# Performance work log

Hardware: AMD Instinct MI355X
Metric: run time of the kernel (lower is better)

Reference implementation:

```python
import jax, jax.numpy as jnp
import numpy as np

B, S, H = 2, 2048, 2048
NQ, NKV = 32, 8
HD = H // NQ  # 64


def setup_inputs() -> dict:
    key = jax.random.key(0)
    ks = jax.random.split(key, 9)
    s = 1.0 / np.sqrt(H)
    return {
        "x": jax.random.normal(ks[0], (B, S, H), dtype=jnp.float32),
        "Wq": jax.random.normal(ks[1], (H, H), dtype=jnp.float32) * s,
        "bq": jnp.zeros((H,), dtype=jnp.float32),
        "Wk": jax.random.normal(ks[2], (H, NKV * HD), dtype=jnp.float32) * s,
        "bk": jnp.zeros((NKV * HD,), dtype=jnp.float32),
        "Wv": jax.random.normal(ks[3], (H, NKV * HD), dtype=jnp.float32) * s,
        "bv": jnp.zeros((NKV * HD,), dtype=jnp.float32),
        "Wo": jax.random.normal(ks[4], (H, H), dtype=jnp.float32) * s,
        "bo": jnp.zeros((H,), dtype=jnp.float32),
    }


def reference(x, Wq, bq, Wk, bk, Wv, bv, Wo, bo):
    Bx, Sx, _ = x.shape
    g = NQ // NKV  # queries per kv head
    q = (x @ Wq + bq).reshape(Bx, Sx, NKV, g, HD)   # grouped query heads
    k = (x @ Wk + bk).reshape(Bx, Sx, NKV, HD)
    v = (x @ Wv + bv).reshape(Bx, Sx, NKV, HD)
    # scores: [B, NKV, g, S, S] -- broadcast KV across group instead of jnp.repeat
    scores = jnp.einsum('bshgd,bkhd->bhgsk', q, k) / jnp.sqrt(jnp.float32(HD))
    probs = jax.nn.softmax(scores, axis=-1)
    out = jnp.einsum('bhgsk,bkhd->bshgd', probs, v).reshape(Bx, Sx, H)
    return out @ Wo + bo
```

## Files before the change

### kernel.cpp

```cpp
#include <hip/hip_runtime.h>
#include <cstdint>
#include <cstddef>

typedef unsigned short u16;
typedef __bf16 bf16x8 __attribute__((ext_vector_type(8)));
typedef float f32x4 __attribute__((ext_vector_type(4)));
typedef unsigned short u16x4 __attribute__((ext_vector_type(4)));
typedef unsigned short u16x8 __attribute__((ext_vector_type(8)));
typedef uint32_t u32x4 __attribute__((ext_vector_type(4)));
typedef __attribute__((address_space(1))) unsigned int as1_uint;
typedef __attribute__((address_space(3))) unsigned int as3_uint;

__device__ __forceinline__ u16 f2bf(float f) {
  uint32_t u = __builtin_bit_cast(uint32_t, f);
  u += 0x7FFFu + ((u >> 16) & 1u);
  return (u16)(u >> 16);
}

__device__ __forceinline__ uint32_t cvtpk2bf(float a, float b) {
  uint32_t r;
  asm("v_cvt_pk_bf16_f32 %0, %1, %2" : "=v"(r) : "v"(a), "v"(b));
  return r;
}

__device__ __forceinline__ float max3f(float a, float b, float c) {
  return fmaxf(fmaxf(a, b), c);
}

__device__ __forceinline__ void gld_lds16(const void* g, void* l) {
  __builtin_amdgcn_global_load_lds((as1_uint*)g, (as3_uint*)l, 16, 0, 0);
}

__global__ __launch_bounds__(256) void k_prep(const float* __restrict__ x,
                                              u16* __restrict__ xb,
                                              const float* __restrict__ Wq,
                                              const float* __restrict__ Wk,
                                              const float* __restrict__ Wv,
                                              const float* __restrict__ Wo,
                                              u16* __restrict__ wqkvT,
                                              u16* __restrict__ woT) {
  constexpr int K = 2048;
  const int z = blockIdx.z;
  if (z >= 4) {
    int i = ((z - 4) * 1024 + blockIdx.y * 32 + blockIdx.x) * 256 + threadIdx.x;
    const float4* p = reinterpret_cast<const float4*>(x) + (size_t)i * 2;
    float4 a = p[0], b = p[1];
    u16x8 r;
    r[0] = f2bf(a.x); r[1] = f2bf(a.y); r[2] = f2bf(a.z); r[3] = f2bf(a.w);
    r[4] = f2bf(b.x); r[5] = f2bf(b.y); r[6] = f2bf(b.z); r[7] = f2bf(b.w);
    *reinterpret_cast<u16x8*>(xb + (size_t)i * 8) = r;
    return;
  }
  const float* W; u16* Wt; int N;
  if (z == 0)      { W = Wq; Wt = wqkvT;                        N = 2048; }
  else if (z == 1) { W = Wo; Wt = woT;                          N = 2048; }
  else if (z == 2) { W = Wk; Wt = wqkvT + (size_t)2048 * 2048;  N = 512;  }
  else             { W = Wv; Wt = wqkvT + (size_t)2560 * 2048;  N = 512;  }
  const int n0 = blockIdx.x * 64;
  if (n0 >= N) return;
  __shared__ u16 tile[64][72];
  const int k0 = blockIdx.y * 64;
  const int r = threadIdx.x >> 4;
  const int c4 = (threadIdx.x & 15) * 4;
#pragma unroll
  for (int i = 0; i < 4; ++i) {
    int kk = r + i * 16;
    float4 v = *reinterpret_cast<const float4*>(W + (size_t)(k0 + kk) * N + n0 + c4);
    tile[kk][c4 + 0] = f2bf(v.x); tile[kk][c4 + 1] = f2bf(v.y);
    tile[kk][c4 + 2] = f2bf(v.z); tile[kk][c4 + 3] = f2bf(v.w);
  }
  __syncthreads();
#pragma unroll
  for (int i = 0; i < 4; ++i) {
    int nn = r + i * 16;
    u16x4 o;
    o[0] = tile[c4 + 0][nn]; o[1] = tile[c4 + 1][nn];
    o[2] = tile[c4 + 2][nn]; o[3] = tile[c4 + 3][nn];
    *reinterpret_cast<u16x4*>(Wt + (size_t)(n0 + nn) * K + k0 + c4) = o;
  }
}

template <bool F32OUT>
__global__ __launch_bounds__(256) void k_gemm(const u16* __restrict__ A,
                                              const u16* __restrict__ Bt,
                                              const float* __restrict__ b0,
                                              const float* __restrict__ b1,
                                              const float* __restrict__ b2,
                                              void* __restrict__ Cout,
                                              int M, int N, int K,
                                              int n1, int n2,
                                              int scaleN, float scaleV,
                                              u16* __restrict__ vout, int vcol0, int ldC) {
  __shared__ __align__(16) u16 As[128 * 64];
  __shared__ __align__(16) u16 Bs[128 * 64];
  const int id = blockIdx.y * gridDim.x + blockIdx.x;
  const int cpx = (gridDim.x * gridDim.y) >> 3;
  const int nid = (id & 7) * cpx + (id >> 3);
  const int m0 = (nid / gridDim.x) * 128, n0 = (nid % gridDim.x) * 128;
  const int tid = threadIdx.x;
  const int l = tid & 63, w = tid >> 6;
  const int wm = w >> 1, wn = w & 1;
  const int lr = l & 15, lo = l >> 4;
  const int srow = w * 8 + (l >> 3);
  const int sc = (l & 7) ^ ((l >> 3) & 7);
  f32x4 acc[4][4] = {};
  for (int kt = 0; kt < K; kt += 64) {
    __syncthreads();
#pragma unroll
    for (int it = 0; it < 4; ++it) {
      int row = it * 32 + srow;
      gld_lds16(A + (size_t)(m0 + row) * K + kt + sc * 8,
                (char*)As + (it * 32 + w * 8) * 128);
      gld_lds16(Bt + (size_t)(n0 + row) * K + kt + sc * 8,
                (char*)Bs + (it * 32 + w * 8) * 128);
    }
    __syncthreads();
    bf16x8 af[4][2], bfr[4][2];
#pragma unroll
    for (int mi = 0; mi < 4; ++mi) {
      int row = wm * 64 + mi * 16 + lr;
#pragma unroll
      for (int ks = 0; ks < 2; ++ks) {
        int ch = (ks * 4 + lo) ^ (row & 7);
        af[mi][ks] = *reinterpret_cast<const bf16x8*>((const char*)As + row * 128 + ch * 16);
      }
    }
#pragma unroll
    for (int nj = 0; nj < 4; ++nj) {
      int row = wn * 64 + nj * 16 + lr;
#pragma unroll
      for (int ks = 0; ks < 2; ++ks) {
        int ch = (ks * 4 + lo) ^ (row & 7);
        bfr[nj][ks] = *reinterpret_cast<const bf16x8*>((const char*)Bs + row * 128 + ch * 16);
      }
    }
#pragma unroll
    for (int mi = 0; mi < 4; ++mi)
#pragma unroll
      for (int nj = 0; nj < 4; ++nj) {
        acc[mi][nj] = __builtin_amdgcn_mfma_f32_16x16x32_bf16(af[mi][0], bfr[nj][0], acc[mi][nj], 0, 0, 0);
        acc[mi][nj] = __builtin_amdgcn_mfma_f32_16x16x32_bf16(af[mi][1], bfr[nj][1], acc[mi][nj], 0, 0, 0);
      }
  }
#pragma unroll
  for (int mi = 0; mi < 4; ++mi) {
    int row = m0 + wm * 64 + mi * 16 + lo * 4;
#pragma unroll
    for (int nj = 0; nj < 4; ++nj) {
      int col = n0 + wn * 64 + nj * 16 + lr;
      float bv = (col < n1) ? b0[col] : (col < n2 ? b1[col - n1] : b2[col - n2]);
      float scc = (col < scaleN) ? scaleV : 1.0f;
      float v[4];
#pragma unroll
      for (int r = 0; r < 4; ++r) v[r] = (acc[mi][nj][r] + bv) * scc;
      if (!F32OUT && col >= vcol0) {
        int d = col - vcol0;
        int kvh = d >> 6, dcol = d & 63;
        int bb = row >> 11, token = row & 2047;
        u16x4 o;
#pragma unroll
        for (int r = 0; r < 4; ++r) o[r] = f2bf(v[r]);
        *reinterpret_cast<u16x4*>(vout + (((size_t)(bb * 8 + kvh) * 64 + dcol) * 2048 + token)) = o;
      } else {
#pragma unroll
        for (int r = 0; r < 4; ++r) {
          if (F32OUT) ((float*)Cout)[(size_t)(row + r) * ldC + col] = v[r];
          else        ((u16*)Cout)[(size_t)(row + r) * ldC + col] = f2bf(v[r]);
        }
      }
    }
  }
}

__global__ __launch_bounds__(512, 4) void k_attn(const u16* __restrict__ QKV,
                                                 const u16* __restrict__ VT,
                                                 u16* __restrict__ Oa) {
  constexpr int S = 2048, LDQ = 2560;
  constexpr float THR = 8.0f;
  __shared__ __align__(16) u16 Ks[2][64 * 64];
  __shared__ __align__(16) u16 Vs[2][64 * 64];
  const int qt = blockIdx.x, h = blockIdx.y, b = blockIdx.z;
  const int kvh = h >> 2;
  const int tid = threadIdx.x, l = tid & 63, w = tid >> 6;
  const int lr = l & 15, lo = l >> 4;
  const size_t base = (size_t)b * S * LDQ;
  const u16* Qg = QKV + base + h * 64;
  const u16* Kg = QKV + base + 2048 + kvh * 64;
  const u16* Vg = VT + (size_t)(b * 8 + kvh) * 64 * 2048;
  const int qrow = qt * 128 + w * 16 + lr;
  const bf16x8 aq0 = *reinterpret_cast<const bf16x8*>(Qg + (size_t)qrow * LDQ + lo * 8);
  const bf16x8 aq1 = *reinterpret_cast<const bf16x8*>(Qg + (size_t)qrow * LDQ + 32 + lo * 8);
  u32x4 onesw; onesw[0] = 0x3F803F80u; onesw[1] = 0x3F803F80u; onesw[2] = 0x3F803F80u; onesw[3] = 0x3F803F80u;
  const bf16x8 ones = __builtin_bit_cast(bf16x8, onesw);
  f32x4 acc[4] = {};
  f32x4 lsum4 = {};
  float mrun = -1e30f;
  const int krow = tid >> 3;
  const int ksc = (l & 7) ^ ((l >> 3) & 7);
  gld_lds16(Kg + (size_t)krow * LDQ + ksc * 8, (char*)Ks[0] + (w * 8) * 128);
  gld_lds16(Vg + (size_t)krow * 2048 + ksc * 8, (char*)Vs[0] + (w * 8) * 128);
  int cur = 0;
  for (int kt = 0; kt < S; kt += 64) {
    __syncthreads();
    if (kt + 64 < S) {
      const int nb = cur ^ 1, nk = kt + 64;
      gld_lds16(Kg + (size_t)(nk + krow) * LDQ + ksc * 8, (char*)Ks[nb] + (w * 8) * 128);
      gld_lds16(Vg + (size_t)krow * 2048 + nk + ksc * 8, (char*)Vs[nb] + (w * 8) * 128);
    }
    float p[16];
    const u16* KsC = Ks[cur];
    __builtin_amdgcn_s_setprio(1);
#pragma unroll
    for (int t = 0; t < 4; ++t) {
      const int row = t * 16 + lr;
      bf16x8 k0 = *reinterpret_cast<const bf16x8*>((const char*)KsC + row * 128 + ((lo ^ (row & 7)) * 16));
      bf16x8 k1 = *reinterpret_cast<const bf16x8*>((const char*)KsC + row * 128 + (((4 + lo) ^ (row & 7)) * 16));
      f32x4 zz = {};
      zz = __builtin_amdgcn_mfma_f32_16x16x32_bf16(k0, aq0, zz, 0, 0, 0);
      zz = __builtin_amdgcn_mfma_f32_16x16x32_bf16(k1, aq1, zz, 0, 0, 0);
#pragma unroll
      for (int r = 0; r < 4; ++r) p[t * 4 + r] = zz[r];
    }
    __builtin_amdgcn_s_setprio(0);
    float m0 = max3f(p[0], p[1], p[2]);
    float m1 = max3f(p[3], p[4], p[5]);
    float m2 = max3f(p[6], p[7], p[8]);
    float m3 = max3f(p[9], p[10], p[11]);
    float m4 = max3f(p[12], p[13], p[14]);
    float tm = fmaxf(max3f(m0, m1, m2), max3f(m3, m4, p[15]));
    tm = fmaxf(tm, __shfl_xor(tm, 16, 64));
    tm = fmaxf(tm, __shfl_xor(tm, 32, 64));
    if (__all(tm <= mrun + THR)) {
#pragma unroll
      for (int i = 0; i < 16; ++i) p[i] = __builtin_amdgcn_exp2f(p[i] - mrun);
    } else {
      float mnew = fmaxf(mrun, tm);
      float alpha = __builtin_amdgcn_exp2f(mrun - mnew);
      mrun = mnew;
#pragma unroll
      for (int i = 0; i < 16; ++i) p[i] = __builtin_amdgcn_exp2f(p[i] - mnew);
#pragma unroll
      for (int r = 0; r < 4; ++r) {
        float ar = __shfl(alpha, lo * 4 + r, 64);
        lsum4[r] *= ar;
#pragma unroll
        for (int nj = 0; nj < 4; ++nj) acc[nj][r] *= ar;
      }
    }
    uint32_t w00 = cvtpk2bf(p[0], p[1]),   w01 = cvtpk2bf(p[2], p[3]);
    uint32_t w10 = cvtpk2bf(p[4], p[5]),   w11 = cvtpk2bf(p[6], p[7]);
    uint32_t w20 = cvtpk2bf(p[8], p[9]),   w21 = cvtpk2bf(p[10], p[11]);
    uint32_t w30 = cvtpk2bf(p[12], p[13]), w31 = cvtpk2bf(p[14], p[15]);
    asm volatile("v_permlane32_swap_b32 %0, %1" : "+v"(w00), "+v"(w10));
    asm volatile("v_permlane16_swap_b32 %0, %1" : "+v"(w00), "+v"(w10));
    asm volatile("v_permlane32_swap_b32 %0, %1" : "+v"(w01), "+v"(w11));
    asm volatile("v_permlane16_swap_b32 %0, %1" : "+v"(w01), "+v"(w11));
    asm volatile("v_permlane32_swap_b32 %0, %1" : "+v"(w20), "+v"(w30));
    asm volatile("v_permlane16_swap_b32 %0, %1" : "+v"(w20), "+v"(w30));
    asm volatile("v_permlane32_swap_b32 %0, %1" : "+v"(w21), "+v"(w31));
    asm volatile("v_permlane16_swap_b32 %0, %1" : "+v"(w21), "+v"(w31));
    u32x4 pq0; pq0[0] = w00; pq0[1] = w01; pq0[2] = w10; pq0[3] = w11;
    u32x4 pq1; pq1[0] = w20; pq1[1] = w21; pq1[2] = w30; pq1[3] = w31;
    const bf16x8 pa0 = __builtin_bit_cast(bf16x8, pq0);
    const bf16x8 pa1 = __builtin_bit_cast(bf16x8, pq1);
    const u16* VsC = Vs[cur];
    __builtin_amdgcn_s_setprio(1);
    lsum4 = __builtin_amdgcn_mfma_f32_16x16x32_bf16(pa0, ones, lsum4, 0, 0, 0);
    lsum4 = __builtin_amdgcn_mfma_f32_16x16x32_bf16(pa1, ones, lsum4, 0, 0, 0);
#pragma unroll
    for (int nj = 0; nj < 4; ++nj) {
      const int vr = nj * 16 + lr;
      const bf16x8 bv0 = *reinterpret_cast<const bf16x8*>((const char*)VsC + vr * 128 + ((lo ^ (vr & 7)) * 16));
      const bf16x8 bv1 = *reinterpret_cast<const bf16x8*>((const char*)VsC + vr * 128 + (((4 + lo) ^ (vr & 7)) * 16));
      acc[nj] = __builtin_amdgcn_mfma_f32_16x16x32_bf16(pa0, bv0, acc[nj], 0, 0, 0);
      acc[nj] = __builtin_amdgcn_mfma_f32_16x16x32_bf16(pa1, bv1, acc[nj], 0, 0, 0);
    }
    __builtin_amdgcn_s_setprio(0);
    cur ^= 1;
  }
  float lf[4];
#pragma unroll
  for (int r = 0; r < 4; ++r) lf[r] = 1.0f / lsum4[r];
  const size_t orow = (size_t)b * S + qt * 128 + w * 16 + lo * 4;
#pragma unroll
  for (int nj = 0; nj < 4; ++nj) {
    const int col = h * 64 + nj * 16 + lr;
#pragma unroll
    for (int r = 0; r < 4; ++r)
      Oa[(orow + r) * 2048 + col] = f2bf(acc[nj][r] * lf[r]);
  }
}

extern "C" void kernel_launch(void* const* d_in, const int* in_sizes, int n_in,
                              void* d_out, int out_size, void* d_ws, size_t ws_size,
                              hipStream_t stream) {
  const float* x  = (const float*)d_in[0];
  const float* Wq = (const float*)d_in[1];
  const float* bq = (const float*)d_in[2];
  const float* Wk = (const float*)d_in[3];
  const float* bk = (const float*)d_in[4];
  const float* Wv = (const float*)d_in[5];
  const float* bv = (const float*)d_in[6];
  const float* Wo = (const float*)d_in[7];
  const float* bo = (const float*)d_in[8];
  float* out = (float*)d_out;
  char* ws = (char*)d_ws;

  u16*   xb    = (u16*)(ws + 0);
  u16*   wqkvT = (u16*)(ws + 16777216);
  u16*   woT   = (u16*)(ws + 29360128);
  u16*   qkv   = (u16*)(ws + 37748736);
  u16*   attn  = (u16*)(ws + 58720256);
  u16*   vtg   = (u16*)(ws + 75497472);

  const float SCL = 0.125f * 1.44269504088896341f;

  k_prep<<<dim3(32, 32, 8), 256, 0, stream>>>(x, xb, Wq, Wk, Wv, Wo, wqkvT, woT);
  k_gemm<false><<<dim3(24, 32), 256, 0, stream>>>(xb, wqkvT, bq, bk, bv, qkv,
                                                  4096, 3072, 2048, 2048, 2560, 2048, SCL,
                                                  vtg, 2560, 2560);
  k_attn<<<dim3(16, 32, 2), 512, 0, stream>>>(qkv, vtg, attn);
  k_gemm<true><<<dim3(16, 32), 256, 0, stream>>>(attn, woT, bo, bo, bo, out,
                                                 4096, 2048, 2048, 2048, 4096, 0, 1.0f,
                                                 nullptr, 1 << 30, 2048);
}
```

Measured before the change: 253.3 us.

## Process 128-key tiles per attention iteration instead of 64

The attention loop now stages two 64-key K/V sub-tiles per double-buffered stage and processes 128 keys per iteration. This halves the number of barriers, online-softmax max reductions and rescale checks per key, and gives more independent MFMA work per iteration. In exchange it doubles LDS use and register pressure, and the launch bounds drop to 2 blocks per CU, which may reduce occupancy and latency hiding.

```diff
diff --git a/kernel.cpp b/kernel.cpp
--- a/kernel.cpp
+++ b/kernel.cpp
@@ -172,13 +172,13 @@
   }
 }
 
-__global__ __launch_bounds__(512, 4) void k_attn(const u16* __restrict__ QKV,
+__global__ __launch_bounds__(512, 2) void k_attn(const u16* __restrict__ QKV,
                                                  const u16* __restrict__ VT,
                                                  u16* __restrict__ Oa) {
   constexpr int S = 2048, LDQ = 2560;
   constexpr float THR = 8.0f;
-  __shared__ __align__(16) u16 Ks[2][64 * 64];
-  __shared__ __align__(16) u16 Vs[2][64 * 64];
+  __shared__ __align__(16) u16 Ks[2][2][64 * 64];
+  __shared__ __align__(16) u16 Vs[2][2][64 * 64];
   const int qt = blockIdx.x, h = blockIdx.y, b = blockIdx.z;
   const int kvh = h >> 2;
   const int tid = threadIdx.x, l = tid & 63, w = tid >> 6;
@@ -197,48 +197,69 @@
   float mrun = -1e30f;
   const int krow = tid >> 3;
   const int ksc = (l & 7) ^ ((l >> 3) & 7);
-  gld_lds16(Kg + (size_t)krow * LDQ + ksc * 8, (char*)Ks[0] + (w * 8) * 128);
-  gld_lds16(Vg + (size_t)krow * 2048 + ksc * 8, (char*)Vs[0] + (w * 8) * 128);
+  gld_lds16(Kg + (size_t)krow * LDQ + ksc * 8,           (char*)Ks[0][0] + (w * 8) * 128);
+  gld_lds16(Kg + (size_t)(64 + krow) * LDQ + ksc * 8,    (char*)Ks[0][1] + (w * 8) * 128);
+  gld_lds16(Vg + (size_t)krow * 2048 + ksc * 8,          (char*)Vs[0][0] + (w * 8) * 128);
+  gld_lds16(Vg + (size_t)krow * 2048 + 64 + ksc * 8,     (char*)Vs[0][1] + (w * 8) * 128);
   int cur = 0;
-  for (int kt = 0; kt < S; kt += 64) {
+  for (int kt = 0; kt < S; kt += 128) {
     __syncthreads();
-    if (kt + 64 < S) {
-      const int nb = cur ^ 1, nk = kt + 64;
-      gld_lds16(Kg + (size_t)(nk + krow) * LDQ + ksc * 8, (char*)Ks[nb] + (w * 8) * 128);
-      gld_lds16(Vg + (size_t)krow * 2048 + nk + ksc * 8, (char*)Vs[nb] + (w * 8) * 128);
-    }
-    float p[16];
-    const u16* KsC = Ks[cur];
+    if (kt + 128 < S) {
+      const int nb = cur ^ 1, nk = kt + 128;
+      gld_lds16(Kg + (size_t)(nk + krow) * LDQ + ksc * 8,        (char*)Ks[nb][0] + (w * 8) * 128);
+      gld_lds16(Kg + (size_t)(nk + 64 + krow) * LDQ + ksc * 8,   (char*)Ks[nb][1] + (w * 8) * 128);
+      gld_lds16(Vg + (size_t)krow * 2048 + nk + ksc * 8,         (char*)Vs[nb][0] + (w * 8) * 128);
+      gld_lds16(Vg + (size_t)krow * 2048 + nk + 64 + ksc * 8,    (char*)Vs[nb][1] + (w * 8) * 128);
+    }
+    float p0[16], p1[16];
+    const u16* K0 = Ks[cur][0];
+    const u16* K1 = Ks[cur][1];
     __builtin_amdgcn_s_setprio(1);
 #pragma unroll
     for (int t = 0; t < 4; ++t) {
       const int row = t * 16 + lr;
-      bf16x8 k0 = *reinterpret_cast<const bf16x8*>((const char*)KsC + row * 128 + ((lo ^ (row & 7)) * 16));
-      bf16x8 k1 = *reinterpret_cast<const bf16x8*>((const char*)KsC + row * 128 + (((4 + lo) ^ (row & 7)) * 16));
-      f32x4 zz = {};
-      zz = __builtin_amdgcn_mfma_f32_16x16x32_bf16(k0, aq0, zz, 0, 0, 0);
-      zz = __builtin_amdgcn_mfma_f32_16x16x32_bf16(k1, aq1, zz, 0, 0, 0);
-#pragma unroll
-      for (int r = 0; r < 4; ++r) p[t * 4 + r] = zz[r];
+      const int c0 = (lo ^ (row & 7)) * 16, c1 = ((4 + lo) ^ (row & 7)) * 16;
+      bf16x8 k00 = *reinterpret_cast<const bf16x8*>((const char*)K0 + row * 128 + c0);
+      bf16x8 k01 = *reinterpret_cast<const bf16x8*>((const char*)K0 + row * 128 + c1);
+      bf16x8 k10 = *reinterpret_cast<const bf16x8*>((const char*)K1 + row * 128 + c0);
+      bf16x8 k11 = *reinterpret_cast<const bf16x8*>((const char*)K1 + row * 128 + c1);
+      f32x4 z0 = {}, z1 = {};
+      z0 = __builtin_amdgcn_mfma_f32_16x16x32_bf16(k00, aq0, z0, 0, 0, 0);
+      z0 = __builtin_amdgcn_mfma_f32_16x16x32_bf16(k01, aq1, z0, 0, 0, 0);
+      z1 = __builtin_amdgcn_mfma_f32_16x16x32_bf16(k10, aq0, z1, 0, 0, 0);
+      z1 = __builtin_amdgcn_mfma_f32_16x16x32_bf16(k11, aq1, z1, 0, 0, 0);
+#pragma unroll
+      for (int r = 0; r < 4; ++r) { p0[t * 4 + r] = z0[r]; p1[t * 4 + r] = z1[r]; }
     }
     __builtin_amdgcn_s_setprio(0);
-    float m0 = max3f(p[0], p[1], p[2]);
-    float m1 = max3f(p[3], p[4], p[5]);
-    float m2 = max3f(p[6], p[7], p[8]);
-    float m3 = max3f(p[9], p[10], p[11]);
-    float m4 = max3f(p[12], p[13], p[14]);
-    float tm = fmaxf(max3f(m0, m1, m2), max3f(m3, m4, p[15]));
-    tm = fmaxf(tm, __shfl_xor(tm, 16, 64));
-    tm = fmaxf(tm, __shfl_xor(tm, 32, 64));
+    float a0 = max3f(p0[0], p0[1], p0[2]);
+    float a1 = max3f(p0[3], p0[4], p0[5]);
+    float a2 = max3f(p0[6], p0[7], p0[8]);
+    float a3 = max3f(p0[9], p0[10], p0[11]);
+    float a4 = max3f(p0[12], p0[13], p0[14]);
+    float tm0 = fmaxf(max3f(a0, a1, a2), max3f(a3, a4, p0[15]));
+    float b0m = max3f(p1[0], p1[1], p1[2]);
+    float b1m = max3f(p1[3], p1[4], p1[5]);
+    float b2m = max3f(p1[6], p1[7], p1[8]);
+    float b3m = max3f(p1[9], p1[10], p1[11]);
+    float b4m = max3f(p1[12], p1[13], p1[14]);
+    float tm1 = fmaxf(max3f(b0m, b1m, b2m), max3f(b3m, b4m, p1[15]));
+    tm0 = fmaxf(tm0, __shfl_xor(tm0, 16, 64));
+    tm1 = fmaxf(tm1, __shfl_xor(tm1, 16, 64));
+    tm0 = fmaxf(tm0, __shfl_xor(tm0, 32, 64));
+    tm1 = fmaxf(tm1, __shfl_xor(tm1, 32, 64));
+    float tm = fmaxf(tm0, tm1);
     if (__all(tm <= mrun + THR)) {
 #pragma unroll
-      for (int i = 0; i < 16; ++i) p[i] = __builtin_amdgcn_exp2f(p[i] - mrun);
+      for (int i = 0; i < 16; ++i) { p0[i] = __builtin_amdgcn_exp2f(p0[i] - mrun);
+                                     p1[i] = __builtin_amdgcn_exp2f(p1[i] - mrun); }
     } else {
       float mnew = fmaxf(mrun, tm);
       float alpha = __builtin_amdgcn_exp2f(mrun - mnew);
       mrun = mnew;
 #pragma unroll
-      for (int i = 0; i < 16; ++i) p[i] = __builtin_amdgcn_exp2f(p[i] - mnew);
+      for (int i = 0; i < 16; ++i) { p0[i] = __builtin_amdgcn_exp2f(p0[i] - mnew);
+                                     p1[i] = __builtin_amdgcn_exp2f(p1[i] - mnew); }
 #pragma unroll
       for (int r = 0; r < 4; ++r) {
         float ar = __shfl(alpha, lo * 4 + r, 64);
@@ -247,10 +268,14 @@
         for (int nj = 0; nj < 4; ++nj) acc[nj][r] *= ar;
       }
     }
-    uint32_t w00 = cvtpk2bf(p[0], p[1]),   w01 = cvtpk2bf(p[2], p[3]);
-    uint32_t w10 = cvtpk2bf(p[4], p[5]),   w11 = cvtpk2bf(p[6], p[7]);
-    uint32_t w20 = cvtpk2bf(p[8], p[9]),   w21 = cvtpk2bf(p[10], p[11]);
-    uint32_t w30 = cvtpk2bf(p[12], p[13]), w31 = cvtpk2bf(p[14], p[15]);
+    uint32_t w00 = cvtpk2bf(p0[0], p0[1]),   w01 = cvtpk2bf(p0[2], p0[3]);
+    uint32_t w10 = cvtpk2bf(p0[4], p0[5]),   w11 = cvtpk2bf(p0[6], p0[7]);
+    uint32_t w20 = cvtpk2bf(p0[8], p0[9]),   w21 = cvtpk2bf(p0[10], p0[11]);
+    uint32_t w30 = cvtpk2bf(p0[12], p0[13]), w31 = cvtpk2bf(p0[14], p0[15]);
+    uint32_t x00 = cvtpk2bf(p1[0], p1[1]),   x01 = cvtpk2bf(p1[2], p1[3]);
+    uint32_t x10 = cvtpk2bf(p1[4], p1[5]),   x11 = cvtpk2bf(p1[6], p1[7]);
+    uint32_t x20 = cvtpk2bf(p1[8], p1[9]),   x21 = cvtpk2bf(p1[10], p1[11]);
+    uint32_t x30 = cvtpk2bf(p1[12], p1[13]), x31 = cvtpk2bf(p1[14], p1[15]);
     asm volatile("v_permlane32_swap_b32 %0, %1" : "+v"(w00), "+v"(w10));
     asm volatile("v_permlane16_swap_b32 %0, %1" : "+v"(w00), "+v"(w10));
     asm volatile("v_permlane32_swap_b32 %0, %1" : "+v"(w01), "+v"(w11));
@@ -259,21 +284,41 @@
     asm volatile("v_permlane16_swap_b32 %0, %1" : "+v"(w20), "+v"(w30));
     asm volatile("v_permlane32_swap_b32 %0, %1" : "+v"(w21), "+v"(w31));
     asm volatile("v_permlane16_swap_b32 %0, %1" : "+v"(w21), "+v"(w31));
+    asm volatile("v_permlane32_swap_b32 %0, %1" : "+v"(x00), "+v"(x10));
+    asm volatile("v_permlane16_swap_b32 %0, %1" : "+v"(x00), "+v"(x10));
+    asm volatile("v_permlane32_swap_b32 %0, %1" : "+v"(x01), "+v"(x11));
+    asm volatile("v_permlane16_swap_b32 %0, %1" : "+v"(x01), "+v"(x11));
+    asm volatile("v_permlane32_swap_b32 %0, %1" : "+v"(x20), "+v"(x30));
+    asm volatile("v_permlane16_swap_b32 %0, %1" : "+v"(x20), "+v"(x30));
+    asm volatile("v_permlane32_swap_b32 %0, %1" : "+v"(x21), "+v"(x31));
+    asm volatile("v_permlane16_swap_b32 %0, %1" : "+v"(x21), "+v"(x31));
     u32x4 pq0; pq0[0] = w00; pq0[1] = w01; pq0[2] = w10; pq0[3] = w11;
     u32x4 pq1; pq1[0] = w20; pq1[1] = w21; pq1[2] = w30; pq1[3] = w31;
+    u32x4 pq2; pq2[0] = x00; pq2[1] = x01; pq2[2] = x10; pq2[3] = x11;
+    u32x4 pq3; pq3[0] = x20; pq3[1] = x21; pq3[2] = x30; pq3[3] = x31;
     const bf16x8 pa0 = __builtin_bit_cast(bf16x8, pq0);
     const bf16x8 pa1 = __builtin_bit_cast(bf16x8, pq1);
-    const u16* VsC = Vs[cur];
+    const bf16x8 pa2 = __builtin_bit_cast(bf16x8, pq2);
+    const bf16x8 pa3 = __builtin_bit_cast(bf16x8, pq3);
+    const u16* V0 = Vs[cur][0];
+    const u16* V1 = Vs[cur][1];
     __builtin_amdgcn_s_setprio(1);
     lsum4 = __builtin_amdgcn_mfma_f32_16x16x32_bf16(pa0, ones, lsum4, 0, 0, 0);
     lsum4 = __builtin_amdgcn_mfma_f32_16x16x32_bf16(pa1, ones, lsum4, 0, 0, 0);
+    lsum4 = __builtin_amdgcn_mfma_f32_16x16x32_bf16(pa2, ones, lsum4, 0, 0, 0);
+    lsum4 = __builtin_amdgcn_mfma_f32_16x16x32_bf16(pa3, ones, lsum4, 0, 0, 0);
 #pragma unroll
     for (int nj = 0; nj < 4; ++nj) {
       const int vr = nj * 16 + lr;
-      const bf16x8 bv0 = *reinterpret_cast<const bf16x8*>((const char*)VsC + vr * 128 + ((lo ^ (vr & 7)) * 16));
-      const bf16x8 bv1 = *reinterpret_cast<const bf16x8*>((const char*)VsC + vr * 128 + (((4 + lo) ^ (vr & 7)) * 16));
-      acc[nj] = __builtin_amdgcn_mfma_f32_16x16x32_bf16(pa0, bv0, acc[nj], 0, 0, 0);
-      acc[nj] = __builtin_amdgcn_mfma_f32_16x16x32_bf16(pa1, bv1, acc[nj], 0, 0, 0);
+      const int c0 = (lo ^ (vr & 7)) * 16, c1 = ((4 + lo) ^ (vr & 7)) * 16;
+      const bf16x8 bv00 = *reinterpret_cast<const bf16x8*>((const char*)V0 + vr * 128 + c0);
+      const bf16x8 bv01 = *reinterpret_cast<const bf16x8*>((const char*)V0 + vr * 128 + c1);
+      const bf16x8 bv10 = *reinterpret_cast<const bf16x8*>((const char*)V1 + vr * 128 + c0);
+      const bf16x8 bv11 = *reinterpret_cast<const bf16x8*>((const char*)V1 + vr * 128 + c1);
+      acc[nj] = __builtin_amdgcn_mfma_f32_16x16x32_bf16(pa0, bv00, acc[nj], 0, 0, 0);
+      acc[nj] = __builtin_amdgcn_mfma_f32_16x16x32_bf16(pa1, bv01, acc[nj], 0, 0, 0);
+      acc[nj] = __builtin_amdgcn_mfma_f32_16x16x32_bf16(pa2, bv10, acc[nj], 0, 0, 0);
+      acc[nj] = __builtin_amdgcn_mfma_f32_16x16x32_bf16(pa3, bv11, acc[nj], 0, 0, 0);
     }
     __builtin_amdgcn_s_setprio(0);
     cur ^= 1;
```

New measurement: 274.8 us. 8.5% more time.
